# Optimization experiments

Measured on AMD Instinct MI355X. Metric: run time of the kernel, lower is better.

## Reference

```python
import jax, jax.numpy as jnp
import numpy as np

N_NODES = 100000
N_EDGES = 1600000
IN_DIM = 256
OUT_DIM = 128


def setup_inputs() -> dict:
    key = jax.random.key(0)
    ks = jax.random.split(key, 8)
    x = jax.random.normal(ks[0], (N_NODES, IN_DIM), dtype=jnp.float32)
    # glorot-ish init scaling
    W = jax.random.normal(ks[1], (IN_DIM, OUT_DIM), dtype=jnp.float32) * (6.0 / (IN_DIM + OUT_DIM)) ** 0.5
    fsW = jax.random.normal(ks[2], (IN_DIM, OUT_DIM), dtype=jnp.float32) * (6.0 / (IN_DIM + OUT_DIM)) ** 0.5
    f_weights = jax.random.normal(ks[3], (2 * OUT_DIM, 1), dtype=jnp.float32) * (6.0 / (2 * OUT_DIM + 1)) ** 0.5
    f_bias = jnp.zeros((1,), dtype=jnp.float32)
    # degrees in [1, 64], strictly positive so pow(deg, -p) is finite
    dia_adj = jax.random.uniform(ks[4], (N_NODES,), dtype=jnp.float32) * 63.0 + 1.0
    row = jax.random.randint(ks[5], (N_EDGES,), 0, N_NODES, dtype=jnp.int32)
    col = jax.random.randint(ks[6], (N_EDGES,), 0, N_NODES, dtype=jnp.int32)
    return {"x": x, "W": W, "fsW": fsW, "f_weights": f_weights,
            "f_bias": f_bias, "dia_adj": dia_adj, "row": row, "col": col}


def reference(x, W, fsW, f_weights, f_bias, dia_adj, row, col):
    # pre_sup = x @ weights_, fpre_sup = x @ fs_weights  (dropout=0, dense inputs)
    pre_sup = x @ W                 # [N, out]
    fpre_sup = x @ fsW              # [N, out]
    d = W.shape[1]
    # concat([vi, vj]) @ f_weights == vi @ f_weights[:d] + vj @ f_weights[d:]
    wi, wj = f_weights[:d], f_weights[d:]
    score = jax.nn.sigmoid(fpre_sup[row] @ wi + fpre_sup[col] @ wj + f_bias)  # [E, 1]
    # degree-power normalization: (deg_i * deg_j) ** (-sigmoid_score)
    deg_vivj = (dia_adj[row] * dia_adj[col])[:, None]                         # [E, 1]
    vals = jnp.power(deg_vivj, -score)[:, 0]                                  # [E]
    # sparse matmul: out[r] += vals_e * pre_sup[c] for each edge e=(r,c)
    msg = vals[:, None] * pre_sup[col]                                        # [E, out]
    out = jax.ops.segment_sum(msg, row, num_segments=x.shape[0])              # [N, out]
    return jax.nn.relu(out)
```

## Files before the change

### kernel.cpp

```cpp
#include <hip/hip_runtime.h>

#define N_NODES 100000
#define N_EDGES 1600000
#define IN_DIM 256
#define OUT_DIM 128
#define BROWS 100
#define NBK 1000
#define PBLK 128
#define EPB 12500

typedef __attribute__((ext_vector_type(4))) float f32x4;
typedef __attribute__((ext_vector_type(8))) short s16x8;

__device__ inline unsigned short f2bf(float f) {
    union { float f; unsigned int u; } a; a.f = f;
    unsigned int r = a.u + 0x7fffu + ((a.u >> 16) & 1u);
    return (unsigned short)(r >> 16);
}
__device__ inline float bf2f(unsigned short h) {
    union { unsigned int u; float f; } a; a.u = ((unsigned int)h) << 16;
    return a.f;
}

__global__ __launch_bounds__(256) void kprep(
        const float* __restrict__ fsW, const float* __restrict__ fw,
        const float* __restrict__ W, const int* __restrict__ row,
        float* __restrict__ u, float* __restrict__ v,
        unsigned short* __restrict__ wt, int* __restrict__ hist_t) {
    __shared__ int h[NBK];
    __shared__ float wi[128], wj[128];
    const int t = threadIdx.x, blk = blockIdx.x;
    if (blk < PBLK) {
        wt[blk * 256 + t] = f2bf(W[(size_t)t * 128 + blk]);
        for (int b = t; b < NBK; b += 256) h[b] = 0;
        __syncthreads();
        const int e0 = blk * EPB;
        for (int i = t; i < EPB; i += 256)
            atomicAdd(&h[row[e0 + i] / BROWS], 1);
        __syncthreads();
        for (int b = t; b < NBK; b += 256)
            hist_t[b * PBLK + blk] = h[b];
    } else {
        if (t < 128) wi[t] = fw[t]; else wj[t - 128] = fw[t];
        __syncthreads();
        const float* rowp = fsW + (size_t)t * OUT_DIM;
        float su = 0.f, sv = 0.f;
        for (int d = 0; d < 128; d += 4) {
            float4 a = *(const float4*)(rowp + d);
            su += a.x * wi[d] + a.y * wi[d + 1] + a.z * wi[d + 2] + a.w * wi[d + 3];
            sv += a.x * wj[d] + a.y * wj[d + 1] + a.z * wj[d + 2] + a.w * wj[d + 3];
        }
        u[t] = su; v[t] = sv;
    }
}

__global__ __launch_bounds__(256) void gemm_mfma(
        const float* __restrict__ x, const unsigned short* __restrict__ wt,
        const float* __restrict__ u, const float* __restrict__ v,
        unsigned short* __restrict__ psb, float* __restrict__ si, float* __restrict__ sj) {
    __shared__ unsigned short xa[64 * 136];

    const int t = threadIdx.x;
    const int wave = t >> 6, lane = t & 63;
    const int l15 = lane & 15, lhi = lane >> 4;
    const int row = t >> 2, quad = t & 3;
    const int brow = blockIdx.x * 64;
    const int gnode = brow + row;
    const bool valid = gnode < N_NODES;

    f32x4 acc[4][2];
#pragma unroll
    for (int mi = 0; mi < 4; ++mi)
#pragma unroll
        for (int ni = 0; ni < 2; ++ni) acc[mi][ni] = (f32x4){0.f, 0.f, 0.f, 0.f};
    float su = 0.f, sv = 0.f;

    const float* xp = x + (size_t)gnode * IN_DIM + quad * 16;
    float4 xr[4];
#pragma unroll
    for (int i = 0; i < 4; ++i) xr[i] = make_float4(0.f, 0.f, 0.f, 0.f);
    if (valid) {
#pragma unroll
        for (int i = 0; i < 4; ++i) xr[i] = ((const float4*)xp)[i];
    }

#pragma unroll
    for (int ph = 0; ph < 4; ++ph) {
        {
            const float* up = u + ph * 64 + quad * 16;
            const float* vp = v + ph * 64 + quad * 16;
            float4 uu0 = ((const float4*)up)[0], uu1 = ((const float4*)up)[1];
            float4 uu2 = ((const float4*)up)[2], uu3 = ((const float4*)up)[3];
            float4 vv0 = ((const float4*)vp)[0], vv1 = ((const float4*)vp)[1];
            float4 vv2 = ((const float4*)vp)[2], vv3 = ((const float4*)vp)[3];
            su = fmaf(xr[0].x, uu0.x, su); su = fmaf(xr[0].y, uu0.y, su);
            su = fmaf(xr[0].z, uu0.z, su); su = fmaf(xr[0].w, uu0.w, su);
            su = fmaf(xr[1].x, uu1.x, su); su = fmaf(xr[1].y, uu1.y, su);
            su = fmaf(xr[1].z, uu1.z, su); su = fmaf(xr[1].w, uu1.w, su);
            su = fmaf(xr[2].x, uu2.x, su); su = fmaf(xr[2].y, uu2.y, su);
            su = fmaf(xr[2].z, uu2.z, su); su = fmaf(xr[2].w, uu2.w, su);
            su = fmaf(xr[3].x, uu3.x, su); su = fmaf(xr[3].y, uu3.y, su);
            su = fmaf(xr[3].z, uu3.z, su); su = fmaf(xr[3].w, uu3.w, su);
            sv = fmaf(xr[0].x, vv0.x, sv); sv = fmaf(xr[0].y, vv0.y, sv);
            sv = fmaf(xr[0].z, vv0.z, sv); sv = fmaf(xr[0].w, vv0.w, sv);
            sv = fmaf(xr[1].x, vv1.x, sv); sv = fmaf(xr[1].y, vv1.y, sv);
            sv = fmaf(xr[1].z, vv1.z, sv); sv = fmaf(xr[1].w, vv1.w, sv);
            sv = fmaf(xr[2].x, vv2.x, sv); sv = fmaf(xr[2].y, vv2.y, sv);
            sv = fmaf(xr[2].z, vv2.z, sv); sv = fmaf(xr[2].w, vv2.w, sv);
            sv = fmaf(xr[3].x, vv3.x, sv); sv = fmaf(xr[3].y, vv3.y, sv);
            sv = fmaf(xr[3].z, vv3.z, sv); sv = fmaf(xr[3].w, vv3.w, sv);
            union { unsigned short h[16]; uint4 q[2]; } pk;
#pragma unroll
            for (int i = 0; i < 4; ++i) {
                pk.h[i * 4 + 0] = f2bf(xr[i].x); pk.h[i * 4 + 1] = f2bf(xr[i].y);
                pk.h[i * 4 + 2] = f2bf(xr[i].z); pk.h[i * 4 + 3] = f2bf(xr[i].w);
            }
            *(uint4*)&xa[row * 72 + quad * 16]     = pk.q[0];
            *(uint4*)&xa[row * 72 + quad * 16 + 8] = pk.q[1];
        }
        if (ph < 3) {
            const float* xpn = xp + (ph + 1) * 64;
            if (valid) {
#pragma unroll
                for (int i = 0; i < 4; ++i) xr[i] = ((const float4*)xpn)[i];
            }
        }
        asm volatile("s_waitcnt lgkmcnt(0)" ::: "memory");
        __builtin_amdgcn_s_barrier();
        {
            const unsigned short* wb0 = wt + (size_t)(wave * 32 + l15) * IN_DIM + ph * 64 + lhi * 8;
            s16x8 bfr[2][2];
#pragma unroll
            for (int ks = 0; ks < 2; ++ks) {
                bfr[ks][0] = *(const s16x8*)(wb0 + ks * 32);
                bfr[ks][1] = *(const s16x8*)(wb0 + (size_t)16 * IN_DIM + ks * 32);
            }
#pragma unroll
            for (int ks = 0; ks < 2; ++ks) {
                const int k0 = ks * 32 + lhi * 8;
                s16x8 afr[4];
#pragma unroll
                for (int mi = 0; mi < 4; ++mi)
                    afr[mi] = *(const s16x8*)&xa[(mi * 16 + l15) * 72 + k0];
#pragma unroll
                for (int mi = 0; mi < 4; ++mi)
#pragma unroll
                    for (int ni = 0; ni < 2; ++ni)
                        acc[mi][ni] = __builtin_amdgcn_mfma_f32_16x16x32_bf16(
                            afr[mi], bfr[ks][ni], acc[mi][ni], 0, 0, 0);
            }
        }
        __builtin_amdgcn_s_barrier();
    }

    su += __shfl_xor(su, 1); su += __shfl_xor(su, 2);
    sv += __shfl_xor(sv, 1); sv += __shfl_xor(sv, 2);
    if (quad == 0 && valid) { si[gnode] = su; sj[gnode] = sv; }

    unsigned short* cl = xa;
#pragma unroll
    for (int mi = 0; mi < 4; ++mi)
#pragma unroll
        for (int ni = 0; ni < 2; ++ni) {
            const int colb = wave * 32 + ni * 16 + l15;
#pragma unroll
            for (int j = 0; j < 4; ++j)
                cl[(mi * 16 + lhi * 4 + j) * 128 + colb] = f2bf(acc[mi][ni][j]);
        }
    __syncthreads();
    {
        const int rl = t >> 2;
        const int cb = (t & 3) * 32;
        if (brow + rl < N_NODES) {
            const uint4* src = (const uint4*)&cl[rl * 128 + cb];
            uint4* dst = (uint4*)&psb[(size_t)(brow + rl) * OUT_DIM + cb];
            dst[0] = src[0]; dst[1] = src[1]; dst[2] = src[2]; dst[3] = src[3];
        }
    }
}

__global__ __launch_bounds__(1024) void kbscan(const int* __restrict__ hist_t,
                                               int* __restrict__ bpre) {
    __shared__ int s[1024];
    const int t = threadIdx.x;
    int v = 0;
    if (t < NBK) {
        const int4* hp = (const int4*)(hist_t + t * PBLK);
#pragma unroll 4
        for (int k = 0; k < PBLK / 4; ++k) {
            int4 a = hp[k];
            v += a.x + a.y + a.z + a.w;
        }
    }
    s[t] = v;
    __syncthreads();
    for (int off = 1; off < 1024; off <<= 1) {
        int nv = (t >= off) ? s[t - off] : 0;
        __syncthreads();
        s[t] += nv;
        __syncthreads();
    }
    if (t < NBK) bpre[t] = s[t] - v;
    if (t == 1023) bpre[NBK] = s[1023];
}

__global__ __launch_bounds__(128) void koff(const int* __restrict__ hist_t,
                                            const int* __restrict__ bpre,
                                            int* __restrict__ off) {
    const int b = blockIdx.x, t = threadIdx.x;
    const int lane = t & 63, w = t >> 6;
    int v = hist_t[b * PBLK + t];
    int s = v;
#pragma unroll
    for (int o = 1; o < 64; o <<= 1) { int tt = __shfl_up(s, o); if (lane >= o) s += tt; }
    __shared__ int ws2[2];
    if (lane == 63) ws2[w] = s;
    __syncthreads();
    int base = (w == 1) ? ws2[0] : 0;
    off[b * PBLK + t] = bpre[b] + base + (s - v);
}

__global__ __launch_bounds__(256) void kpart1(const int* __restrict__ row,
                                              const int* __restrict__ col,
                                              const int* __restrict__ off,
                                              unsigned int* __restrict__ part) {
    __shared__ int cur[NBK];
    const int t = threadIdx.x, blk = blockIdx.x;
    for (int b = t; b < NBK; b += 256) cur[b] = off[b * PBLK + blk];
    __syncthreads();
    const int e0 = blk * EPB;
    for (int i = t; i < EPB; i += 256) {
        int r = row[e0 + i], c = col[e0 + i];
        int b = r / BROWS;
        int rl = r - b * BROWS;
        int pos = atomicAdd(&cur[b], 1);
        part[pos] = ((unsigned)rl << 17) | (unsigned)c;
    }
}

__global__ __launch_bounds__(256) void kpart2(const unsigned int* __restrict__ part,
                                              const int* __restrict__ bpre,
                                              const float* __restrict__ si,
                                              const float* __restrict__ sj,
                                              const float* __restrict__ dia,
                                              const float* __restrict__ fb,
                                              int2* __restrict__ epack,
                                              int* __restrict__ offs,
                                              int* __restrict__ deg) {
    __shared__ int cnt[BROWS];
    __shared__ int cur[BROWS];
    __shared__ float sil[BROWS], dial[BROWS];
    __shared__ int wtot[4];
    const int b = blockIdx.x, t = threadIdx.x;
    const int rbase = b * BROWS;
    if (t < BROWS) {
        cnt[t] = 0;
        sil[t] = si[rbase + t];
        dial[t] = dia[rbase + t];
    }
    __syncthreads();
    const int bstart = bpre[b], bend = bpre[b + 1];
    for (int e = bstart + t; e < bend; e += 256)
        atomicAdd(&cnt[part[e] >> 17], 1);
    __syncthreads();
    {
        int vv = (t < BROWS) ? cnt[t] : 0;
        int lane = t & 63, w = t >> 6;
        int s = vv;
#pragma unroll
        for (int o = 1; o < 64; o <<= 1) { int tt = __shfl_up(s, o); if (lane >= o) s += tt; }
        if (lane == 63) wtot[w] = s;
        __syncthreads();
        int base = 0;
        for (int k = 0; k < w; ++k) base += wtot[k];
        int excl = base + s - vv;
        if (t < BROWS) {
            cur[t] = bstart + excl;
            offs[rbase + t] = bstart + excl;
            deg[rbase + t] = vv;
        }
    }
    __syncthreads();
    const float fbv = fb[0];
    for (int e = bstart + t; e < bend; e += 256) {
        unsigned pk = part[e];
        int rl = (int)(pk >> 17);
        int c = (int)(pk & 0x1FFFFu);
        float tval = sil[rl] + sj[c] + fbv;
        float sg = 1.f / (1.f + expf(-tval));
        float l2 = log2f(dial[rl] * dia[c]);
        float val = exp2f(-sg * l2);
        int pos = atomicAdd(&cur[rl], 1);
        epack[pos] = make_int2(c, __float_as_int(val));
    }
}

__global__ __launch_bounds__(256) void kgather(
        const int* __restrict__ offs, const int* __restrict__ deg,
        const int2* __restrict__ epack,
        const unsigned short* __restrict__ psb, float* __restrict__ out) {
    int lane = threadIdx.x & 31;
    int node = blockIdx.x * 8 + (threadIdx.x >> 5);
    if (node >= N_NODES) return;
    int start = offs[node], d = deg[node];
    const int2* ep = epack + start;
    float a0 = 0.f, a1 = 0.f, a2 = 0.f, a3 = 0.f;
    int k = 0;
    for (; k + 8 <= d; k += 8) {
        int2 e0 = ep[k],     e1 = ep[k + 1], e2 = ep[k + 2], e3 = ep[k + 3];
        int2 e4 = ep[k + 4], e5 = ep[k + 5], e6 = ep[k + 6], e7 = ep[k + 7];
        ushort4 p0 = *(const ushort4*)&psb[(size_t)e0.x * OUT_DIM + lane * 4];
        ushort4 p1 = *(const ushort4*)&psb[(size_t)e1.x * OUT_DIM + lane * 4];
        ushort4 p2 = *(const ushort4*)&psb[(size_t)e2.x * OUT_DIM + lane * 4];
        ushort4 p3 = *(const ushort4*)&psb[(size_t)e3.x * OUT_DIM + lane * 4];
        ushort4 p4 = *(const ushort4*)&psb[(size_t)e4.x * OUT_DIM + lane * 4];
        ushort4 p5 = *(const ushort4*)&psb[(size_t)e5.x * OUT_DIM + lane * 4];
        ushort4 p6 = *(const ushort4*)&psb[(size_t)e6.x * OUT_DIM + lane * 4];
        ushort4 p7 = *(const ushort4*)&psb[(size_t)e7.x * OUT_DIM + lane * 4];
        float v0 = __int_as_float(e0.y), v1 = __int_as_float(e1.y);
        float v2 = __int_as_float(e2.y), v3 = __int_as_float(e3.y);
        float v4 = __int_as_float(e4.y), v5 = __int_as_float(e5.y);
        float v6 = __int_as_float(e6.y), v7 = __int_as_float(e7.y);
        a0 = fmaf(v0, bf2f(p0.x), a0); a1 = fmaf(v0, bf2f(p0.y), a1);
        a2 = fmaf(v0, bf2f(p0.z), a2); a3 = fmaf(v0, bf2f(p0.w), a3);
        a0 = fmaf(v1, bf2f(p1.x), a0); a1 = fmaf(v1, bf2f(p1.y), a1);
        a2 = fmaf(v1, bf2f(p1.z), a2); a3 = fmaf(v1, bf2f(p1.w), a3);
        a0 = fmaf(v2, bf2f(p2.x), a0); a1 = fmaf(v2, bf2f(p2.y), a1);
        a2 = fmaf(v2, bf2f(p2.z), a2); a3 = fmaf(v2, bf2f(p2.w), a3);
        a0 = fmaf(v3, bf2f(p3.x), a0); a1 = fmaf(v3, bf2f(p3.y), a1);
        a2 = fmaf(v3, bf2f(p3.z), a2); a3 = fmaf(v3, bf2f(p3.w), a3);
        a0 = fmaf(v4, bf2f(p4.x), a0); a1 = fmaf(v4, bf2f(p4.y), a1);
        a2 = fmaf(v4, bf2f(p4.z), a2); a3 = fmaf(v4, bf2f(p4.w), a3);
        a0 = fmaf(v5, bf2f(p5.x), a0); a1 = fmaf(v5, bf2f(p5.y), a1);
        a2 = fmaf(v5, bf2f(p5.z), a2); a3 = fmaf(v5, bf2f(p5.w), a3);
        a0 = fmaf(v6, bf2f(p6.x), a0); a1 = fmaf(v6, bf2f(p6.y), a1);
        a2 = fmaf(v6, bf2f(p6.z), a2); a3 = fmaf(v6, bf2f(p6.w), a3);
        a0 = fmaf(v7, bf2f(p7.x), a0); a1 = fmaf(v7, bf2f(p7.y), a1);
        a2 = fmaf(v7, bf2f(p7.z), a2); a3 = fmaf(v7, bf2f(p7.w), a3);
    }
    for (; k < d; ++k) {
        int2 e0 = ep[k];
        float v0 = __int_as_float(e0.y);
        ushort4 p0 = *(const ushort4*)&psb[(size_t)e0.x * OUT_DIM + lane * 4];
        a0 = fmaf(v0, bf2f(p0.x), a0);
        a1 = fmaf(v0, bf2f(p0.y), a1);
        a2 = fmaf(v0, bf2f(p0.z), a2);
        a3 = fmaf(v0, bf2f(p0.w), a3);
    }
    float4 o;
    o.x = fmaxf(a0, 0.f); o.y = fmaxf(a1, 0.f);
    o.z = fmaxf(a2, 0.f); o.w = fmaxf(a3, 0.f);
    *(float4*)&out[(size_t)node * OUT_DIM + lane * 4] = o;
}

extern "C" void kernel_launch(void* const* d_in, const int* in_sizes, int n_in,
                              void* d_out, int out_size, void* d_ws, size_t ws_size,
                              hipStream_t stream) {
    const float* x   = (const float*)d_in[0];
    const float* W   = (const float*)d_in[1];
    const float* fsW = (const float*)d_in[2];
    const float* fw  = (const float*)d_in[3];
    const float* fb  = (const float*)d_in[4];
    const float* dia = (const float*)d_in[5];
    const int*   row = (const int*)d_in[6];
    const int*   col = (const int*)d_in[7];
    float* out = (float*)d_out;

    char* p = (char*)d_ws;
    auto alloc = [&](size_t bytes) -> char* {
        char* r = p; p += (bytes + 255) & ~(size_t)255; return r;
    };
    float* u      = (float*)alloc(256 * 4);
    float* v      = (float*)alloc(256 * 4);
    unsigned short* wtb = (unsigned short*)alloc((size_t)128 * 256 * 2);
    float* si     = (float*)alloc((size_t)N_NODES * 4);
    float* sj     = (float*)alloc((size_t)N_NODES * 4);
    int*   deg    = (int*)alloc((size_t)N_NODES * 4);
    int*   offs   = (int*)alloc((size_t)N_NODES * 4);
    unsigned short* psb = (unsigned short*)alloc((size_t)N_NODES * OUT_DIM * 2);
    int*   hist_t = (int*)alloc((size_t)NBK * PBLK * 4);
    int*   bpre   = (int*)alloc((size_t)(NBK + 1) * 4);
    int*   off    = (int*)alloc((size_t)NBK * PBLK * 4);
    unsigned int* part = (unsigned int*)alloc((size_t)N_EDGES * 4);
    int2*  epack  = (int2*)alloc((size_t)N_EDGES * 8);

    kprep<<<PBLK + 1, 256, 0, stream>>>(fsW, fw, W, row, u, v, wtb, hist_t);
    gemm_mfma<<<(N_NODES + 63) / 64, 256, 0, stream>>>(x, wtb, u, v, psb, si, sj);
    kbscan<<<1, 1024, 0, stream>>>(hist_t, bpre);
    koff<<<NBK, PBLK, 0, stream>>>(hist_t, bpre, off);
    kpart1<<<PBLK, 256, 0, stream>>>(row, col, off, part);
    kpart2<<<NBK, 256, 0, stream>>>(part, bpre, si, sj, dia, fb, epack, offs, deg);
    kgather<<<N_NODES / 8, 256, 0, stream>>>(offs, deg, epack, psb, out);
}
```

Measured before the change: 200.9 us.

## Fuse edge partition pass into GEMM launch as extra blocks for concurrency

The edge bucketing kernel (kpart1) becomes the first 128 blocks of the GEMM launch, so partitioning runs alongside the node GEMM instead of serially. The scan kernels now run before the GEMM so the offsets are ready. This removes one launch and fills the device during the small partition pass. The partition blocks reuse the GEMM's shared buffer for the cursors, which adds shared-memory footprint to those blocks, and the scan kernels now delay the start of the GEMM.

Result: faster. 186.4 us (median of 2 runs) (-7.2%).

```diff
diff --git a/kernel.cpp b/kernel.cpp
--- a/kernel.cpp
+++ b/kernel.cpp
@@ -54,18 +54,78 @@
     }
 }
 
-__global__ __launch_bounds__(256) void gemm_mfma(
+__global__ __launch_bounds__(1024) void kbscan(const int* __restrict__ hist_t,
+                                               int* __restrict__ bpre) {
+    __shared__ int s[1024];
+    const int t = threadIdx.x;
+    int v = 0;
+    if (t < NBK) {
+        const int4* hp = (const int4*)(hist_t + t * PBLK);
+#pragma unroll 4
+        for (int k = 0; k < PBLK / 4; ++k) {
+            int4 a = hp[k];
+            v += a.x + a.y + a.z + a.w;
+        }
+    }
+    s[t] = v;
+    __syncthreads();
+    for (int off = 1; off < 1024; off <<= 1) {
+        int nv = (t >= off) ? s[t - off] : 0;
+        __syncthreads();
+        s[t] += nv;
+        __syncthreads();
+    }
+    if (t < NBK) bpre[t] = s[t] - v;
+    if (t == 1023) bpre[NBK] = s[1023];
+}
+
+__global__ __launch_bounds__(128) void koff(const int* __restrict__ hist_t,
+                                            const int* __restrict__ bpre,
+                                            int* __restrict__ off) {
+    const int b = blockIdx.x, t = threadIdx.x;
+    const int lane = t & 63, w = t >> 6;
+    int v = hist_t[b * PBLK + t];
+    int s = v;
+#pragma unroll
+    for (int o = 1; o < 64; o <<= 1) { int tt = __shfl_up(s, o); if (lane >= o) s += tt; }
+    __shared__ int ws2[2];
+    if (lane == 63) ws2[w] = s;
+    __syncthreads();
+    int base = (w == 1) ? ws2[0] : 0;
+    off[b * PBLK + t] = bpre[b] + base + (s - v);
+}
+
+__global__ __launch_bounds__(256) void gpart(
         const float* __restrict__ x, const unsigned short* __restrict__ wt,
         const float* __restrict__ u, const float* __restrict__ v,
-        unsigned short* __restrict__ psb, float* __restrict__ si, float* __restrict__ sj) {
+        unsigned short* __restrict__ psb, float* __restrict__ si, float* __restrict__ sj,
+        const int* __restrict__ row, const int* __restrict__ col,
+        const int* __restrict__ off, unsigned int* __restrict__ part) {
     __shared__ unsigned short xa[64 * 136];
 
     const int t = threadIdx.x;
+
+    if (blockIdx.x < PBLK) {
+        int* cur = (int*)xa;
+        const int blk = blockIdx.x;
+        for (int b = t; b < NBK; b += 256) cur[b] = off[b * PBLK + blk];
+        __syncthreads();
+        const int e0 = blk * EPB;
+        for (int i = t; i < EPB; i += 256) {
+            int r = row[e0 + i], c = col[e0 + i];
+            int b = r / BROWS;
+            int rl = r - b * BROWS;
+            int pos = atomicAdd(&cur[b], 1);
+            part[pos] = ((unsigned)rl << 17) | (unsigned)c;
+        }
+        return;
+    }
+
     const int wave = t >> 6, lane = t & 63;
     const int l15 = lane & 15, lhi = lane >> 4;
-    const int row = t >> 2, quad = t & 3;
-    const int brow = blockIdx.x * 64;
-    const int gnode = brow + row;
+    const int rw = t >> 2, quad = t & 3;
+    const int brow = (blockIdx.x - PBLK) * 64;
+    const int gnode = brow + rw;
     const bool valid = gnode < N_NODES;
 
     f32x4 acc[4][2];
@@ -115,8 +175,8 @@
                 pk.h[i * 4 + 0] = f2bf(xr[i].x); pk.h[i * 4 + 1] = f2bf(xr[i].y);
                 pk.h[i * 4 + 2] = f2bf(xr[i].z); pk.h[i * 4 + 3] = f2bf(xr[i].w);
             }
-            *(uint4*)&xa[row * 72 + quad * 16]     = pk.q[0];
-            *(uint4*)&xa[row * 72 + quad * 16 + 8] = pk.q[1];
+            *(uint4*)&xa[rw * 72 + quad * 16]     = pk.q[0];
+            *(uint4*)&xa[rw * 72 + quad * 16 + 8] = pk.q[1];
         }
         if (ph < 3) {
             const float* xpn = xp + (ph + 1) * 64;
@@ -176,65 +236,6 @@
             uint4* dst = (uint4*)&psb[(size_t)(brow + rl) * OUT_DIM + cb];
             dst[0] = src[0]; dst[1] = src[1]; dst[2] = src[2]; dst[3] = src[3];
         }
-    }
-}
-
-__global__ __launch_bounds__(1024) void kbscan(const int* __restrict__ hist_t,
-                                               int* __restrict__ bpre) {
-    __shared__ int s[1024];
-    const int t = threadIdx.x;
-    int v = 0;
-    if (t < NBK) {
-        const int4* hp = (const int4*)(hist_t + t * PBLK);
-#pragma unroll 4
-        for (int k = 0; k < PBLK / 4; ++k) {
-            int4 a = hp[k];
-            v += a.x + a.y + a.z + a.w;
-        }
-    }
-    s[t] = v;
-    __syncthreads();
-    for (int off = 1; off < 1024; off <<= 1) {
-        int nv = (t >= off) ? s[t - off] : 0;
-        __syncthreads();
-        s[t] += nv;
-        __syncthreads();
-    }
-    if (t < NBK) bpre[t] = s[t] - v;
-    if (t == 1023) bpre[NBK] = s[1023];
-}
-
-__global__ __launch_bounds__(128) void koff(const int* __restrict__ hist_t,
-                                            const int* __restrict__ bpre,
-                                            int* __restrict__ off) {
-    const int b = blockIdx.x, t = threadIdx.x;
-    const int lane = t & 63, w = t >> 6;
-    int v = hist_t[b * PBLK + t];
-    int s = v;
-#pragma unroll
-    for (int o = 1; o < 64; o <<= 1) { int tt = __shfl_up(s, o); if (lane >= o) s += tt; }
-    __shared__ int ws2[2];
-    if (lane == 63) ws2[w] = s;
-    __syncthreads();
-    int base = (w == 1) ? ws2[0] : 0;
-    off[b * PBLK + t] = bpre[b] + base + (s - v);
-}
-
-__global__ __launch_bounds__(256) void kpart1(const int* __restrict__ row,
-                                              const int* __restrict__ col,
-                                              const int* __restrict__ off,
-                                              unsigned int* __restrict__ part) {
-    __shared__ int cur[NBK];
-    const int t = threadIdx.x, blk = blockIdx.x;
-    for (int b = t; b < NBK; b += 256) cur[b] = off[b * PBLK + blk];
-    __syncthreads();
-    const int e0 = blk * EPB;
-    for (int i = t; i < EPB; i += 256) {
-        int r = row[e0 + i], c = col[e0 + i];
-        int b = r / BROWS;
-        int rl = r - b * BROWS;
-        int pos = atomicAdd(&cur[b], 1);
-        part[pos] = ((unsigned)rl << 17) | (unsigned)c;
     }
 }
 
@@ -385,10 +386,10 @@
     int2*  epack  = (int2*)alloc((size_t)N_EDGES * 8);
 
     kprep<<<PBLK + 1, 256, 0, stream>>>(fsW, fw, W, row, u, v, wtb, hist_t);
-    gemm_mfma<<<(N_NODES + 63) / 64, 256, 0, stream>>>(x, wtb, u, v, psb, si, sj);
     kbscan<<<1, 1024, 0, stream>>>(hist_t, bpre);
     koff<<<NBK, PBLK, 0, stream>>>(hist_t, bpre, off);
-    kpart1<<<PBLK, 256, 0, stream>>>(row, col, off, part);
+    gpart<<<PBLK + (N_NODES + 63) / 64, 256, 0, stream>>>(
+        x, wtb, u, v, psb, si, sj, row, col, off, part);
     kpart2<<<NBK, 256, 0, stream>>>(part, bpre, si, sj, dia, fb, epack, offs, deg);
     kgather<<<N_NODES / 8, 256, 0, stream>>>(offs, deg, epack, psb, out);
 }
```
